# Kernel tuning notes

Measured on AMD Instinct MI355X. Metric: run time of the kernel, lower is better.

## Reference

```python
import jax, jax.numpy as jnp
import numpy as np

D_H, D_G, D_PROJ = 1280, 768, 256
SCALE = D_PROJ ** (-0.5)

def setup_inputs() -> dict:
    key = jax.random.key(0)
    k1, k2, k3, k4 = jax.random.split(key, 4)
    B, L, T = 8, 4096, 512
    H = jax.random.normal(k1, (B, L, D_H), dtype=jnp.float32)
    G = jax.random.normal(k2, (B, T, D_G), dtype=jnp.float32)
    attn_mask = jnp.zeros((B, L), dtype=bool)  # True = pad/ignore
    # nn.Linear weights: (out_features, in_features)
    Wk = jax.random.normal(k3, (D_PROJ, D_H), dtype=jnp.float32) * (D_H ** -0.5)
    Wq = jax.random.normal(k4, (D_PROJ, D_G), dtype=jnp.float32) * (D_G ** -0.5)
    return {"H": H, "G": G, "attn_mask": attn_mask, "Wk": Wk, "Wq": Wq}

def reference(H, G, attn_mask, Wk, Wq):
    # K = Wk(H): (B,L,P); Q = Wq(G): (B,T,P)
    K = jnp.einsum('bld,pd->blp', H, Wk)
    Q = jnp.einsum('btd,pd->btp', G, Wq)
    # scores (B,T,L); streaming two-pass softmax in the original is exactly
    # softmax over L -> compute it stably in one fused expression here.
    logits = jnp.einsum('btp,blp->btl', Q, K) * SCALE
    logits = jnp.where(attn_mask[:, None, :], -jnp.inf, logits)
    alpha = jax.nn.softmax(logits, axis=-1)
    Z = jnp.einsum('btl,bld->btd', alpha, H)  # (B,T,Dh)
    return Z
```

## Files before the change

### kernel.cpp

```cpp
#include <hip/hip_runtime.h>
#include <hip/hip_bf16.h>
#include <stdint.h>


typedef float f32x4 __attribute__((ext_vector_type(4)));
typedef short bf16x8 __attribute__((ext_vector_type(8)));

__device__ __forceinline__ unsigned short f2bf(float f) {
    union { float f; uint32_t u; } v; v.f = f;
    uint32_t u = v.u;
    u += 0x7fffu + ((u >> 16) & 1u);
    return (unsigned short)(u >> 16);
}
__device__ __forceinline__ float bf2f(unsigned short h) {
    union { uint32_t u; float f; } v; v.u = ((uint32_t)h) << 16;
    return v.f;
}

template<bool AF32, bool BF32, bool OBF16>
__global__ __launch_bounds__(256)
void gemm_bt(const void* __restrict__ Ap, const void* __restrict__ Bp,
             void* __restrict__ Cp, int M, int N, int K,
             long sA, long sB, long sC, float scale)
{
    constexpr int PK = 40;
    __shared__ __align__(16) unsigned short lA[128 * PK];
    __shared__ __align__(16) unsigned short lB[128 * PK];

    const int mt = M >> 7;
    const int tm = blockIdx.x % mt;
    const int tn = blockIdx.x / mt;
    const int b  = blockIdx.y;
    const int tid = threadIdx.x;
    const int lane = tid & 63, wv = tid >> 6;
    const int wr = wv >> 1, wc = wv & 1;
    const int fr = lane & 15, fk = lane >> 4;

    f32x4 acc[4][4] = {};

    const char* Abase = (const char*)Ap;
    const char* Bbase = (const char*)Bp;

    for (int k0 = 0; k0 < K; k0 += 32) {
        if constexpr (AF32) {
            const float* A = (const float*)Abase + (long)b * sA + (long)tm * 128 * K + k0;
            #pragma unroll
            for (int it = 0; it < 4; ++it) {
                int chunk = it * 256 + tid;
                int row = chunk >> 3;
                int kc  = (chunk & 7) << 2;
                const float4 v = *(const float4*)(A + (long)row * K + kc);
                ushort4 w;
                w.x = f2bf(v.x); w.y = f2bf(v.y); w.z = f2bf(v.z); w.w = f2bf(v.w);
                *(ushort4*)(&lA[row * PK + kc]) = w;
            }
        } else {
            const unsigned short* A = (const unsigned short*)Abase + (long)b * sA + (long)tm * 128 * K + k0;
            #pragma unroll
            for (int it = 0; it < 2; ++it) {
                int chunk = it * 256 + tid;
                int row = chunk >> 2;
                int kc  = (chunk & 3) << 3;
                *(uint4*)(&lA[row * PK + kc]) = *(const uint4*)(A + (long)row * K + kc);
            }
        }
        if constexpr (BF32) {
            const float* B = (const float*)Bbase + (long)b * sB + (long)tn * 128 * K + k0;
            #pragma unroll
            for (int it = 0; it < 4; ++it) {
                int chunk = it * 256 + tid;
                int row = chunk >> 3;
                int kc  = (chunk & 7) << 2;
                const float4 v = *(const float4*)(B + (long)row * K + kc);
                ushort4 w;
                w.x = f2bf(v.x); w.y = f2bf(v.y); w.z = f2bf(v.z); w.w = f2bf(v.w);
                *(ushort4*)(&lB[row * PK + kc]) = w;
            }
        } else {
            const unsigned short* B = (const unsigned short*)Bbase + (long)b * sB + (long)tn * 128 * K + k0;
            #pragma unroll
            for (int it = 0; it < 2; ++it) {
                int chunk = it * 256 + tid;
                int row = chunk >> 2;
                int kc  = (chunk & 3) << 3;
                *(uint4*)(&lB[row * PK + kc]) = *(const uint4*)(B + (long)row * K + kc);
            }
        }
        __syncthreads();
        bf16x8 af[4], bfr[4];
        #pragma unroll
        for (int i = 0; i < 4; ++i)
            af[i] = *(const bf16x8*)(&lA[(wr * 64 + i * 16 + fr) * PK + fk * 8]);
        #pragma unroll
        for (int i = 0; i < 4; ++i)
            bfr[i] = *(const bf16x8*)(&lB[(wc * 64 + i * 16 + fr) * PK + fk * 8]);
        #pragma unroll
        for (int mi = 0; mi < 4; ++mi)
            #pragma unroll
            for (int ni = 0; ni < 4; ++ni)
                acc[mi][ni] = __builtin_amdgcn_mfma_f32_16x16x32_bf16(af[mi], bfr[ni], acc[mi][ni], 0, 0, 0);
        __syncthreads();
    }

    if constexpr (OBF16) {
        unsigned short* C = (unsigned short*)Cp + (long)b * sC + ((long)tm * 128) * N + (long)tn * 128;
        #pragma unroll
        for (int mi = 0; mi < 4; ++mi)
            #pragma unroll
            for (int ni = 0; ni < 4; ++ni)
                #pragma unroll
                for (int j = 0; j < 4; ++j) {
                    int m = wr * 64 + mi * 16 + fk * 4 + j;
                    int n = wc * 64 + ni * 16 + fr;
                    C[(long)m * N + n] = f2bf(acc[mi][ni][j] * scale);
                }
    } else {
        float* C = (float*)Cp + (long)b * sC + ((long)tm * 128) * N + (long)tn * 128;
        #pragma unroll
        for (int mi = 0; mi < 4; ++mi)
            #pragma unroll
            for (int ni = 0; ni < 4; ++ni)
                #pragma unroll
                for (int j = 0; j < 4; ++j) {
                    int m = wr * 64 + mi * 16 + fk * 4 + j;
                    int n = wc * 64 + ni * 16 + fr;
                    C[(long)m * N + n] = acc[mi][ni][j] * scale;
                }
    }
}

__global__ __launch_bounds__(256)
void gemm_kn(const unsigned short* __restrict__ Ap, const float* __restrict__ Bp,
             float* __restrict__ Cp, int M, int N, int K,
             long sA, long sB, long sC)
{
    constexpr int PK = 40;
    __shared__ __align__(16) unsigned short lA[128 * PK];
    __shared__ __align__(16) unsigned short lB[128 * PK];

    const int mt = M >> 7;
    const int tm = blockIdx.x % mt;
    const int tn = blockIdx.x / mt;
    const int b  = blockIdx.y;
    const int tid = threadIdx.x;
    const int lane = tid & 63, wv = tid >> 6;
    const int wr = wv >> 1, wc = wv & 1;
    const int fr = lane & 15, fk = lane >> 4;

    f32x4 acc[4][4] = {};

    const unsigned short* A0 = Ap + (long)b * sA + (long)tm * 128 * K;
    const int nn = tid & 127;
    const int half = tid >> 7;

    for (int k0 = 0; k0 < K; k0 += 32) {
        #pragma unroll
        for (int it = 0; it < 2; ++it) {
            int chunk = it * 256 + tid;
            int row = chunk >> 2;
            int kc  = (chunk & 3) << 3;
            *(uint4*)(&lA[row * PK + kc]) = *(const uint4*)(A0 + (long)row * K + k0 + kc);
        }
        {
            const float* Bb = Bp + (long)b * sB + ((long)(k0 + half * 16)) * N + (long)tn * 128 + nn;
            unsigned short t16[16];
            #pragma unroll
            for (int kk = 0; kk < 16; ++kk)
                t16[kk] = f2bf(Bb[(long)kk * N]);
            *(uint4*)(&lB[nn * PK + half * 16 + 0]) = *(uint4*)(&t16[0]);
            *(uint4*)(&lB[nn * PK + half * 16 + 8]) = *(uint4*)(&t16[8]);
        }
        __syncthreads();
        bf16x8 af[4], bfr[4];
        #pragma unroll
        for (int i = 0; i < 4; ++i)
            af[i] = *(const bf16x8*)(&lA[(wr * 64 + i * 16 + fr) * PK + fk * 8]);
        #pragma unroll
        for (int i = 0; i < 4; ++i)
            bfr[i] = *(const bf16x8*)(&lB[(wc * 64 + i * 16 + fr) * PK + fk * 8]);
        #pragma unroll
        for (int mi = 0; mi < 4; ++mi)
            #pragma unroll
            for (int ni = 0; ni < 4; ++ni)
                acc[mi][ni] = __builtin_amdgcn_mfma_f32_16x16x32_bf16(af[mi], bfr[ni], acc[mi][ni], 0, 0, 0);
        __syncthreads();
    }

    float* C = Cp + (long)b * sC + ((long)tm * 128) * N + (long)tn * 128;
    #pragma unroll
    for (int mi = 0; mi < 4; ++mi)
        #pragma unroll
        for (int ni = 0; ni < 4; ++ni)
            #pragma unroll
            for (int j = 0; j < 4; ++j) {
                int m = wr * 64 + mi * 16 + fk * 4 + j;
                int n = wc * 64 + ni * 16 + fr;
                C[(long)m * N + n] = acc[mi][ni][j];
            }
}

__global__ __launch_bounds__(256)
void softmax_rows(unsigned short* __restrict__ S, const unsigned char* __restrict__ mask)
{
    const int row = blockIdx.x;
    const int b = row >> 9;
    const long base = (long)row * 4096;
    const int tid = threadIdx.x, lane = tid & 63, wv = tid >> 6;
    __shared__ float red[8];

    uint4 s0 = *(const uint4*)(S + base + tid * 16);
    uint4 s1 = *(const uint4*)(S + base + tid * 16 + 8);
    uint4 mv = *(const uint4*)(mask + (long)b * 4096 + tid * 16);
    const unsigned char* mb = (const unsigned char*)&mv;

    unsigned int words[8] = { s0.x, s0.y, s0.z, s0.w, s1.x, s1.y, s1.z, s1.w };
    float x[16];
    #pragma unroll
    for (int i = 0; i < 8; ++i) {
        x[2 * i]     = bf2f((unsigned short)(words[i] & 0xffffu));
        x[2 * i + 1] = bf2f((unsigned short)(words[i] >> 16));
    }
    #pragma unroll
    for (int i = 0; i < 16; ++i)
        if (mb[i]) x[i] = -1e30f;

    float m = x[0];
    #pragma unroll
    for (int i = 1; i < 16; ++i) m = fmaxf(m, x[i]);
    #pragma unroll
    for (int off = 32; off; off >>= 1) m = fmaxf(m, __shfl_xor(m, off));
    if (lane == 0) red[wv] = m;
    __syncthreads();
    m = fmaxf(fmaxf(red[0], red[1]), fmaxf(red[2], red[3]));

    float p[16];
    float s = 0.f;
    #pragma unroll
    for (int i = 0; i < 16; ++i) { p[i] = __expf(x[i] - m); s += p[i]; }
    #pragma unroll
    for (int off = 32; off; off >>= 1) s += __shfl_xor(s, off);
    if (lane == 0) red[4 + wv] = s;
    __syncthreads();
    s = (red[4] + red[5]) + (red[6] + red[7]);
    const float inv = 1.0f / s;

    unsigned int ow[8];
    #pragma unroll
    for (int i = 0; i < 8; ++i) {
        unsigned int lo = f2bf(p[2 * i] * inv);
        unsigned int hi = f2bf(p[2 * i + 1] * inv);
        ow[i] = lo | (hi << 16);
    }
    uint4 o0 = { ow[0], ow[1], ow[2], ow[3] };
    uint4 o1 = { ow[4], ow[5], ow[6], ow[7] };
    *(uint4*)(S + base + tid * 16)     = o0;
    *(uint4*)(S + base + tid * 16 + 8) = o1;
}

extern "C" void kernel_launch(void* const* d_in, const int* in_sizes, int n_in,
                              void* d_out, int out_size, void* d_ws, size_t ws_size,
                              hipStream_t stream)
{
    const float*         H    = (const float*)d_in[0];
    const float*         G    = (const float*)d_in[1];
    const unsigned char* mask = (const unsigned char*)d_in[2];
    const float*         Wk   = (const float*)d_in[3];
    const float*         Wq   = (const float*)d_in[4];
    float*               out  = (float*)d_out;

    unsigned short* Kb = (unsigned short*)d_ws;
    unsigned short* Qb = Kb + (long)8 * 4096 * 256;
    unsigned short* Sb = Qb + (long)8 * 512 * 256;

    gemm_bt<true, true, true><<<dim3(512, 1), 256, 0, stream>>>(
        H, Wk, Kb, 32768, 256, 1280, 0, 0, 0, 1.0f);
    gemm_bt<true, true, true><<<dim3(64, 1), 256, 0, stream>>>(
        G, Wq, Qb, 4096, 256, 768, 0, 0, 0, 1.0f);
    gemm_bt<false, false, true><<<dim3(128, 8), 256, 0, stream>>>(
        Qb, Kb, Sb, 512, 4096, 256,
        (long)512 * 256, (long)4096 * 256, (long)512 * 4096, 0.0625f);
    softmax_rows<<<dim3(4096), 256, 0, stream>>>(Sb, mask);
    gemm_kn<<<dim3(40, 8), 256, 0, stream>>>(
        Sb, H, out, 512, 1280, 4096,
        (long)512 * 4096, (long)4096 * 1280, (long)512 * 1280);
}
```

Measured before the change: 270.5 us.

## Swizzle LDS layout, XCD-aware block remap, halve gemm_kn N-tile for more blocks

Replaces the padded LDS indexing with an XOR swizzle of the 8-element k-chunk by row group in all GEMMs. Block indices are remapped so consecutive tiles land on the same XCD. In the projection GEMMs, N-tiles vary fastest so blocks sharing an A tile run together. The final alpha·H GEMM uses a 128x64 tile, doubling its grid from 320 to 640 blocks to fill more CUs. The bf16 conversion now uses the HIP intrinsic. Smaller tiles lower per-block reuse, and the remap assumes grid sizes divisible by 8.

```diff
diff --git a/kernel.cpp b/kernel.cpp
--- a/kernel.cpp
+++ b/kernel.cpp
@@ -7,29 +7,36 @@
 typedef short bf16x8 __attribute__((ext_vector_type(8)));
 
 __device__ __forceinline__ unsigned short f2bf(float f) {
-    union { float f; uint32_t u; } v; v.f = f;
-    uint32_t u = v.u;
-    u += 0x7fffu + ((u >> 16) & 1u);
-    return (unsigned short)(u >> 16);
+    __hip_bfloat16 h = __float2bfloat16(f);
+    return __builtin_bit_cast(unsigned short, h);
 }
 __device__ __forceinline__ float bf2f(unsigned short h) {
     union { uint32_t u; float f; } v; v.u = ((uint32_t)h) << 16;
     return v.f;
 }
 
-template<bool AF32, bool BF32, bool OBF16>
+__device__ __forceinline__ int xcdswz(int bx, int nbx) {
+    int cpx = nbx >> 3;
+    return (bx & 7) * cpx + (bx >> 3);
+}
+
+__device__ __forceinline__ int lidx(int row, int kshort) {
+    return row * 40 + (((kshort >> 3) ^ ((row >> 3) & 3)) << 3) + (kshort & 7);
+}
+
+template<bool AF32, bool BF32, bool OBF16, bool TNF>
 __global__ __launch_bounds__(256)
 void gemm_bt(const void* __restrict__ Ap, const void* __restrict__ Bp,
              void* __restrict__ Cp, int M, int N, int K,
              long sA, long sB, long sC, float scale)
 {
-    constexpr int PK = 40;
-    __shared__ __align__(16) unsigned short lA[128 * PK];
-    __shared__ __align__(16) unsigned short lB[128 * PK];
-
-    const int mt = M >> 7;
-    const int tm = blockIdx.x % mt;
-    const int tn = blockIdx.x / mt;
+    __shared__ __align__(16) unsigned short lA[128 * 40];
+    __shared__ __align__(16) unsigned short lB[128 * 40];
+
+    const int bx = xcdswz(blockIdx.x, gridDim.x);
+    const int mt = M >> 7, nt = N >> 7;
+    const int tm = TNF ? (bx / nt) : (bx % mt);
+    const int tn = TNF ? (bx % nt) : (bx / mt);
     const int b  = blockIdx.y;
     const int tid = threadIdx.x;
     const int lane = tid & 63, wv = tid >> 6;
@@ -52,7 +59,7 @@
                 const float4 v = *(const float4*)(A + (long)row * K + kc);
                 ushort4 w;
                 w.x = f2bf(v.x); w.y = f2bf(v.y); w.z = f2bf(v.z); w.w = f2bf(v.w);
-                *(ushort4*)(&lA[row * PK + kc]) = w;
+                *(ushort4*)(&lA[lidx(row, kc)]) = w;
             }
         } else {
             const unsigned short* A = (const unsigned short*)Abase + (long)b * sA + (long)tm * 128 * K + k0;
@@ -61,7 +68,7 @@
                 int chunk = it * 256 + tid;
                 int row = chunk >> 2;
                 int kc  = (chunk & 3) << 3;
-                *(uint4*)(&lA[row * PK + kc]) = *(const uint4*)(A + (long)row * K + kc);
+                *(uint4*)(&lA[lidx(row, kc)]) = *(const uint4*)(A + (long)row * K + kc);
             }
         }
         if constexpr (BF32) {
@@ -74,7 +81,7 @@
                 const float4 v = *(const float4*)(B + (long)row * K + kc);
                 ushort4 w;
                 w.x = f2bf(v.x); w.y = f2bf(v.y); w.z = f2bf(v.z); w.w = f2bf(v.w);
-                *(ushort4*)(&lB[row * PK + kc]) = w;
+                *(ushort4*)(&lB[lidx(row, kc)]) = w;
             }
         } else {
             const unsigned short* B = (const unsigned short*)Bbase + (long)b * sB + (long)tn * 128 * K + k0;
@@ -83,17 +90,17 @@
                 int chunk = it * 256 + tid;
                 int row = chunk >> 2;
                 int kc  = (chunk & 3) << 3;
-                *(uint4*)(&lB[row * PK + kc]) = *(const uint4*)(B + (long)row * K + kc);
+                *(uint4*)(&lB[lidx(row, kc)]) = *(const uint4*)(B + (long)row * K + kc);
             }
         }
         __syncthreads();
         bf16x8 af[4], bfr[4];
         #pragma unroll
         for (int i = 0; i < 4; ++i)
-            af[i] = *(const bf16x8*)(&lA[(wr * 64 + i * 16 + fr) * PK + fk * 8]);
+            af[i] = *(const bf16x8*)(&lA[lidx(wr * 64 + i * 16 + fr, fk * 8)]);
         #pragma unroll
         for (int i = 0; i < 4; ++i)
-            bfr[i] = *(const bf16x8*)(&lB[(wc * 64 + i * 16 + fr) * PK + fk * 8]);
+            bfr[i] = *(const bf16x8*)(&lB[lidx(wc * 64 + i * 16 + fr, fk * 8)]);
         #pragma unroll
         for (int mi = 0; mi < 4; ++mi)
             #pragma unroll
@@ -134,24 +141,24 @@
              float* __restrict__ Cp, int M, int N, int K,
              long sA, long sB, long sC)
 {
-    constexpr int PK = 40;
-    __shared__ __align__(16) unsigned short lA[128 * PK];
-    __shared__ __align__(16) unsigned short lB[128 * PK];
-
+    __shared__ __align__(16) unsigned short lA[128 * 40];
+    __shared__ __align__(16) unsigned short lB[64 * 40];
+
+    const int bx = xcdswz(blockIdx.x, gridDim.x);
     const int mt = M >> 7;
-    const int tm = blockIdx.x % mt;
-    const int tn = blockIdx.x / mt;
+    const int tm = bx % mt;
+    const int tn = bx / mt;
     const int b  = blockIdx.y;
     const int tid = threadIdx.x;
     const int lane = tid & 63, wv = tid >> 6;
     const int wr = wv >> 1, wc = wv & 1;
     const int fr = lane & 15, fk = lane >> 4;
 
-    f32x4 acc[4][4] = {};
+    f32x4 acc[4][2] = {};
 
     const unsigned short* A0 = Ap + (long)b * sA + (long)tm * 128 * K;
-    const int nn = tid & 127;
-    const int half = tid >> 7;
+    const int nn    = tid & 63;
+    const int khalf = tid >> 6;
 
     for (int k0 = 0; k0 < K; k0 += 32) {
         #pragma unroll
@@ -159,42 +166,41 @@
             int chunk = it * 256 + tid;
             int row = chunk >> 2;
             int kc  = (chunk & 3) << 3;
-            *(uint4*)(&lA[row * PK + kc]) = *(const uint4*)(A0 + (long)row * K + k0 + kc);
+            *(uint4*)(&lA[lidx(row, kc)]) = *(const uint4*)(A0 + (long)row * K + k0 + kc);
         }
         {
-            const float* Bb = Bp + (long)b * sB + ((long)(k0 + half * 16)) * N + (long)tn * 128 + nn;
-            unsigned short t16[16];
-            #pragma unroll
-            for (int kk = 0; kk < 16; ++kk)
-                t16[kk] = f2bf(Bb[(long)kk * N]);
-            *(uint4*)(&lB[nn * PK + half * 16 + 0]) = *(uint4*)(&t16[0]);
-            *(uint4*)(&lB[nn * PK + half * 16 + 8]) = *(uint4*)(&t16[8]);
-        }
-        __syncthreads();
-        bf16x8 af[4], bfr[4];
+            const float* Bb = Bp + (long)b * sB + (long)(k0 + khalf * 8) * N + (long)tn * 64 + nn;
+            unsigned short t8[8];
+            #pragma unroll
+            for (int kk = 0; kk < 8; ++kk)
+                t8[kk] = f2bf(Bb[(long)kk * N]);
+            *(uint4*)(&lB[lidx(nn, khalf * 8)]) = *(uint4*)(&t8[0]);
+        }
+        __syncthreads();
+        bf16x8 af[4], bfr[2];
         #pragma unroll
         for (int i = 0; i < 4; ++i)
-            af[i] = *(const bf16x8*)(&lA[(wr * 64 + i * 16 + fr) * PK + fk * 8]);
-        #pragma unroll
-        for (int i = 0; i < 4; ++i)
-            bfr[i] = *(const bf16x8*)(&lB[(wc * 64 + i * 16 + fr) * PK + fk * 8]);
-        #pragma unroll
-        for (int mi = 0; mi < 4; ++mi)
-            #pragma unroll
-            for (int ni = 0; ni < 4; ++ni)
+            af[i] = *(const bf16x8*)(&lA[lidx(wr * 64 + i * 16 + fr, fk * 8)]);
+        #pragma unroll
+        for (int i = 0; i < 2; ++i)
+            bfr[i] = *(const bf16x8*)(&lB[lidx(wc * 32 + i * 16 + fr, fk * 8)]);
+        #pragma unroll
+        for (int mi = 0; mi < 4; ++mi)
+            #pragma unroll
+            for (int ni = 0; ni < 2; ++ni)
                 acc[mi][ni] = __builtin_amdgcn_mfma_f32_16x16x32_bf16(af[mi], bfr[ni], acc[mi][ni], 0, 0, 0);
         __syncthreads();
     }
 
-    float* C = Cp + (long)b * sC + ((long)tm * 128) * N + (long)tn * 128;
+    float* C = Cp + (long)b * sC + ((long)tm * 128) * N + (long)tn * 64;
     #pragma unroll
     for (int mi = 0; mi < 4; ++mi)
         #pragma unroll
-        for (int ni = 0; ni < 4; ++ni)
+        for (int ni = 0; ni < 2; ++ni)
             #pragma unroll
             for (int j = 0; j < 4; ++j) {
                 int m = wr * 64 + mi * 16 + fk * 4 + j;
-                int n = wc * 64 + ni * 16 + fr;
+                int n = wc * 32 + ni * 16 + fr;
                 C[(long)m * N + n] = acc[mi][ni][j];
             }
 }
@@ -272,15 +278,15 @@
     unsigned short* Qb = Kb + (long)8 * 4096 * 256;
     unsigned short* Sb = Qb + (long)8 * 512 * 256;
 
-    gemm_bt<true, true, true><<<dim3(512, 1), 256, 0, stream>>>(
+    gemm_bt<true, true, true, true><<<dim3(512, 1), 256, 0, stream>>>(
         H, Wk, Kb, 32768, 256, 1280, 0, 0, 0, 1.0f);
-    gemm_bt<true, true, true><<<dim3(64, 1), 256, 0, stream>>>(
+    gemm_bt<true, true, true, true><<<dim3(64, 1), 256, 0, stream>>>(
         G, Wq, Qb, 4096, 256, 768, 0, 0, 0, 1.0f);
-    gemm_bt<false, false, true><<<dim3(128, 8), 256, 0, stream>>>(
+    gemm_bt<false, false, true, false><<<dim3(128, 8), 256, 0, stream>>>(
         Qb, Kb, Sb, 512, 4096, 256,
         (long)512 * 256, (long)4096 * 256, (long)512 * 4096, 0.0625f);
     softmax_rows<<<dim3(4096), 256, 0, stream>>>(Sb, mask);
-    gemm_kn<<<dim3(40, 8), 256, 0, stream>>>(
+    gemm_kn<<<dim3(80, 8), 256, 0, stream>>>(
         Sb, H, out, 512, 1280, 4096,
         (long)512 * 4096, (long)4096 * 1280, (long)512 * 1280);
 }
```

Result: faster. 243.5 us (-10.0%).
